# Kernel tuning notes

Measured on AMD Instinct MI355X. Metric: run time of the kernel, lower is better.

## Reference

```python
import jax, jax.numpy as jnp
import numpy as np

C = 128
B = 64
EPS = 1e-6


def _ln2d(x, w, b):
    # LayerNorm over channel dim (NAFNet-style LayerNorm2d), eps=1e-6
    mu = x.mean(axis=1, keepdims=True)
    var = ((x - mu) ** 2).mean(axis=1, keepdims=True)
    return (x - mu) / jnp.sqrt(var + EPS) * w[None, :, None, None] + b[None, :, None, None]


def _conv4(x, w, b):
    # Conv2d kernel 4, stride 4, no padding; NCHW / OIHW
    y = jax.lax.conv_general_dilated(x, w, (4, 4), 'VALID',
                                     dimension_numbers=('NCHW', 'OIHW', 'NCHW'))
    return y + b[None, :, None, None]


def _pixel_shuffle4(x):
    # (B, c*16, H, W) -> (B, c, 4H, 4W), torch PixelShuffle semantics
    b, c16, h, w = x.shape
    c = c16 // 16
    x = x.reshape(b, c, 4, 4, h, w)
    x = x.transpose(0, 1, 4, 2, 5, 3)
    return x.reshape(b, c, h * 4, w * 4)


def setup_inputs() -> dict:
    key = jax.random.key(0)
    ks = jax.random.split(key, 16)
    s = 0.02
    return {
        'x_l': jax.random.normal(ks[0], (B, C, 32, 32), jnp.float32),
        'x_r': jax.random.normal(ks[1], (B, C, 32, 32), jnp.float32),
        'ln_w_l': jnp.ones((C,), jnp.float32), 'ln_b_l': jnp.zeros((C,), jnp.float32),
        'ln_w_r': jnp.ones((C,), jnp.float32), 'ln_b_r': jnp.zeros((C,), jnp.float32),
        'Wl1': jax.random.normal(ks[2], (C, C, 4, 4), jnp.float32) * s,
        'bl1': jnp.zeros((C,), jnp.float32),
        'Wr1': jax.random.normal(ks[3], (C, C, 4, 4), jnp.float32) * s,
        'br1': jnp.zeros((C,), jnp.float32),
        'Wl2': jax.random.normal(ks[4], (C, C, 4, 4), jnp.float32) * s,
        'bl2': jnp.zeros((C,), jnp.float32),
        'Wr2': jax.random.normal(ks[5], (C, C, 4, 4), jnp.float32) * s,
        'br2': jnp.zeros((C,), jnp.float32),
        'pos': jax.random.normal(ks[6], (1, C, 8, 8), jnp.float32),
        'beta': jax.random.normal(ks[7], (1, C, 1, 1), jnp.float32) * s,
        'gamma': jax.random.normal(ks[8], (1, C, 1, 1), jnp.float32) * s,
        'Wl3': jax.random.normal(ks[9], (16 * C, C), jnp.float32) * s,
        'bl3': jnp.zeros((16 * C,), jnp.float32),
        'Wr3': jax.random.normal(ks[10], (16 * C, C), jnp.float32) * s,
        'br3': jnp.zeros((16 * C,), jnp.float32),
    }


def reference(x_l, x_r, ln_w_l, ln_b_l, ln_w_r, ln_b_r, Wl1, bl1, Wr1, br1,
              Wl2, bl2, Wr2, br2, pos, beta, gamma, Wl3, bl3, Wr3, br3):
    c = x_l.shape[1]
    scale = c ** (-0.5)
    B1 = x_l.shape[0]
    B2 = x_r.shape[0]

    Ql = _conv4(_ln2d(x_l, ln_w_l, ln_b_l), Wl1, bl1) + pos  # (B1,c,8,8)
    Qr = _conv4(_ln2d(x_r, ln_w_r, ln_b_r), Wr1, br1) + pos  # (B2,c,8,8)
    h1, w1 = Ql.shape[-2], Ql.shape[-1]
    h2, w2 = Qr.shape[-2], Qr.shape[-1]
    m1, m2 = h1 * w1, h2 * w2

    Qlm = Ql.transpose(0, 2, 3, 1).reshape(B1, m1, c)          # b (h w) c
    Qrm = Qr.transpose(1, 0, 2, 3).reshape(c, B2 * m2)         # c (b h w)
    Vl = (_conv4(x_l, Wl2, bl2) + pos).transpose(0, 2, 3, 1).reshape(B1 * m1, c)
    Vr = (_conv4(x_r, Wr2, br2) + pos).transpose(0, 2, 3, 1).reshape(B2 * m2, c)

    attn = jnp.matmul(Qlm, Qrm) * scale                        # (B1, m1, B2*m2)

    F_r2l = jnp.matmul(jax.nn.softmax(attn * (B2 ** (-0.5)), axis=-1), Vr)
    F_r2l = F_r2l.reshape(B1, h1, w1, c)

    attn2 = attn.reshape(B1, m1, B2, m2).transpose(2, 3, 0, 1).reshape(B2, m2, B1 * m1)
    F_l2r = jnp.matmul(jax.nn.softmax(attn2 * (B1 ** (-0.5)), axis=-1), Vl)
    F_l2r = F_l2r.reshape(B2, h2, w2, c)

    F_r2l = _pixel_shuffle4((jnp.matmul(F_r2l, Wl3.T) + bl3).transpose(0, 3, 1, 2)) * beta
    F_l2r = _pixel_shuffle4((jnp.matmul(F_l2r, Wr3.T) + br3).transpose(0, 3, 1, 2)) * gamma
    return (x_l + F_r2l, x_r + F_l2r)
```

## Files before the change

### kernel.cpp

```cpp
#include <hip/hip_runtime.h>
#include <stdint.h>

using bf16x8 = __attribute__((ext_vector_type(8))) short;
using f32x4  = __attribute__((ext_vector_type(4))) float;

__device__ __forceinline__ unsigned short f2bf(float f) {
  union { float f; uint32_t u; } v; v.f = f;
  uint32_t r = v.u + 0x7FFFu + ((v.u >> 16) & 1u);
  return (unsigned short)(r >> 16);
}
__device__ __forceinline__ uint32_t pk2(float a, float b) {
  return (uint32_t)f2bf(a) | ((uint32_t)f2bf(b) << 16);
}
__device__ __forceinline__ float bf2f(unsigned short s) {
  union { uint32_t u; float f; } v; v.u = ((uint32_t)s) << 16;
  return v.f;
}
__device__ __forceinline__ f32x4 mfma16(bf16x8 a, bf16x8 b, f32x4 c) {
  return __builtin_amdgcn_mfma_f32_16x16x32_bf16(a, b, c, 0, 0, 0);
}

__global__ __launch_bounds__(256) void k_lnstats(
    const float* __restrict__ xl, const float* __restrict__ xr,
    float* __restrict__ muW, float* __restrict__ rsW)
{
  const int bx = blockIdx.x;
  const int side = bx >> 7, rem = bx & 127;
  const int b = rem >> 1, half = rem & 1;
  const float* x = (side ? xr : xl) + (size_t)b * 131072 + half * 512;
  const int t = threadIdx.x;
  const int px = t * 2;
  float s0=0, s1=0, q0=0, q1=0;
#pragma unroll 4
  for (int c = 0; c < 128; ++c) {
    const float2 v = *(const float2*)(x + c*1024 + px);
    s0 += v.x; q0 += v.x*v.x;
    s1 += v.y; q1 += v.y*v.y;
  }
  const int o = (side*64 + b)*1024 + half*512 + px;
  float2 mu, rs;
  mu.x = s0*(1.0f/128.0f); mu.y = s1*(1.0f/128.0f);
  rs.x = rsqrtf(fmaxf(q0*(1.0f/128.0f) - mu.x*mu.x, 0.0f) + 1e-6f);
  rs.y = rsqrtf(fmaxf(q1*(1.0f/128.0f) - mu.y*mu.y, 0.0f) + 1e-6f);
  *(float2*)(muW + o) = mu;
  *(float2*)(rsW + o) = rs;
}

__global__ __launch_bounds__(256) void k_wprep(
    const float* __restrict__ lnwl, const float* __restrict__ lnbl,
    const float* __restrict__ lnwr, const float* __restrict__ lnbr,
    const float* __restrict__ Wl1, const float* __restrict__ bl1,
    const float* __restrict__ Wr1, const float* __restrict__ br1,
    const float* __restrict__ Wl2, const float* __restrict__ Wr2,
    unsigned short* __restrict__ Wq, unsigned short* __restrict__ Wv,
    float* __restrict__ bqW)
{
  const int bx = blockIdx.x;
  const int side = bx >> 7, co = bx & 127;
  const float* W1  = side ? Wr1 : Wl1;
  const float* W2  = side ? Wr2 : Wl2;
  const float* b1  = side ? br1 : bl1;
  const float* lnw = side ? lnwr : lnwl;
  const float* lnb = side ? lnbr : lnbl;
  const int t = threadIdx.x;
  const int ci = t >> 1;
  const float lw = lnw[ci], lb = lnb[ci];

  const size_t dsto = (size_t)(side*32 + (t>>3))*8192 + (size_t)co*64 + (t&7)*8;

  const float* src1 = W1 + (size_t)co*2048 + t*8;
  const float4 a0 = *(const float4*)(src1);
  const float4 a1 = *(const float4*)(src1 + 4);
  float part = (a0.x+a0.y+a0.z+a0.w + a1.x+a1.y+a1.z+a1.w) * lb;
  uint4 pkq;
  pkq.x = pk2(a0.x*lw, a0.y*lw); pkq.y = pk2(a0.z*lw, a0.w*lw);
  pkq.z = pk2(a1.x*lw, a1.y*lw); pkq.w = pk2(a1.z*lw, a1.w*lw);
  *(uint4*)(Wq + dsto) = pkq;

  const float* src2 = W2 + (size_t)co*2048 + t*8;
  const float4 c0 = *(const float4*)(src2);
  const float4 c1 = *(const float4*)(src2 + 4);
  uint4 pkv;
  pkv.x = pk2(c0.x, c0.y); pkv.y = pk2(c0.z, c0.w);
  pkv.z = pk2(c1.x, c1.y); pkv.w = pk2(c1.z, c1.w);
  *(uint4*)(Wv + dsto) = pkv;

  __shared__ float red[4];
  float v = part;
  v += __shfl_down(v, 32, 64); v += __shfl_down(v, 16, 64);
  v += __shfl_down(v, 8, 64);  v += __shfl_down(v, 4, 64);
  v += __shfl_down(v, 2, 64);  v += __shfl_down(v, 1, 64);
  if ((t & 63) == 0) red[t >> 6] = v;
  __syncthreads();
  if (t == 0) bqW[side*128 + co] = b1[co] + red[0] + red[1] + red[2] + red[3];
}

__global__ __launch_bounds__(256) void k_conv(
    const float* __restrict__ xl, const float* __restrict__ xr,
    const unsigned short* __restrict__ Wq, const unsigned short* __restrict__ Wv,
    const float* __restrict__ muW, const float* __restrict__ rsW,
    unsigned short* __restrict__ Cpart)
{
  const int bid = blockIdx.x;
  const int ks = bid & 3;
  const int img = (bid >> 2) & 63;
  const int ctype = bid >> 8;
  const int side = ctype & 1;
  const bool isQ = ctype < 2;
  const float* x = (side ? xr : xl) + (size_t)img * 131072;
  const unsigned short* Bsrc = (isQ ? Wq : Wv) + (size_t)side * 262144;

  const int t = threadIdx.x;
  const int w = t >> 6, l = t & 63, lo = l & 15, g = l >> 4;

  __shared__ __align__(16) unsigned char lds[24576];
  unsigned char* A = lds;
  unsigned char* B = lds + 8192;

  const int cl   = t >> 6;
  const int px0  = (t & 63) * 16;
  const int y    = px0 >> 5;
  const int wr   = y & 3;
  const int pbase = (y >> 2)*8 + ((px0 & 31) >> 2);

  float4 mu4[4], rs4[4];
  if (isQ) {
    const int o = (side*64 + img)*1024 + px0;
#pragma unroll
    for (int i = 0; i < 4; ++i) {
      mu4[i] = *(const float4*)(muW + o + 4*i);
      rs4[i] = *(const float4*)(rsW + o + 4*i);
    }
  }

  const int cout = t >> 1, part = t & 1;
  const int keyB = ((cout ^ (cout >> 3)) & 7) << 4;

  f32x4 acc[4][2];
#pragma unroll
  for (int a = 0; a < 4; ++a) { acc[a][0] = (f32x4)0.0f; acc[a][1] = (f32x4)0.0f; }

  for (int it = 0; it < 8; ++it) {
    const int kb = ks*8 + it;
    __syncthreads();
    {
      const float* xs = x + (size_t)(kb*4 + cl)*1024 + px0;
#pragma unroll
      for (int i = 0; i < 4; ++i) {
        float4 v = *(const float4*)(xs + 4*i);
        if (isQ) {
          v.x = (v.x - mu4[i].x)*rs4[i].x; v.y = (v.y - mu4[i].y)*rs4[i].y;
          v.z = (v.z - mu4[i].z)*rs4[i].z; v.w = (v.w - mu4[i].w)*rs4[i].w;
        }
        const int p = pbase + i;
        int dst = p*128 + cl*32 + wr*8;
        dst ^= ((p ^ (p >> 3)) & 7) << 4;
        *(uint2*)(A + dst) = make_uint2(pk2(v.x, v.y), pk2(v.z, v.w));
      }
    }
    {
      const unsigned short* bs = Bsrc + (size_t)kb*8192 + t*32;
#pragma unroll
      for (int i = 0; i < 4; ++i) {
        const bf16x8 v = *(const bf16x8*)(bs + i*8);
        *(bf16x8*)(B + cout*128 + ((part*64 + i*16) ^ keyB)) = v;
      }
    }
    __syncthreads();
    bf16x8 af[4][2], bfr[2][2];
#pragma unroll
    for (int mf = 0; mf < 4; ++mf) {
      const int row = mf*16 + lo;
      const int key = ((row ^ (row >> 3)) & 7) << 4;
#pragma unroll
      for (int kc = 0; kc < 2; ++kc)
        af[mf][kc] = *(const bf16x8*)(A + row*128 + ((kc*64 + g*16) ^ key));
    }
#pragma unroll
    for (int nf = 0; nf < 2; ++nf) {
      const int row = w*32 + nf*16 + lo;
      const int key = ((row ^ (row >> 3)) & 7) << 4;
#pragma unroll
      for (int kc = 0; kc < 2; ++kc)
        bfr[nf][kc] = *(const bf16x8*)(B + row*128 + ((kc*64 + g*16) ^ key));
    }
    __builtin_amdgcn_s_setprio(1);
#pragma unroll
    for (int kc = 0; kc < 2; ++kc)
#pragma unroll
      for (int nf = 0; nf < 2; ++nf)
#pragma unroll
        for (int mf = 0; mf < 4; ++mf)
          acc[mf][nf] = mfma16(af[mf][kc], bfr[nf][kc], acc[mf][nf]);
    __builtin_amdgcn_s_setprio(0);
  }

  unsigned short* Cp = Cpart + (size_t)bid * 8192;
#pragma unroll
  for (int mf = 0; mf < 4; ++mf)
#pragma unroll
    for (int nf = 0; nf < 2; ++nf) {
      const int c = w*32 + nf*16 + lo;
      const int p0 = mf*16 + g*4;
      *(uint2*)(Cp + c*64 + p0) =
          make_uint2(pk2(acc[mf][nf][0], acc[mf][nf][1]),
                     pk2(acc[mf][nf][2], acc[mf][nf][3]));
    }
}

__global__ __launch_bounds__(256) void k_convred(
    const unsigned short* __restrict__ Cpart,
    const float* __restrict__ bqW,
    const float* __restrict__ bl2, const float* __restrict__ br2,
    const float* __restrict__ pos,
    unsigned short* __restrict__ Qbf, unsigned short* __restrict__ Vtbf)
{
  const int bid2 = blockIdx.x;
  const int ctype = bid2 >> 6, img = bid2 & 63;
  const int side = ctype & 1;
  const bool isQ = ctype < 2;
  const int t = threadIdx.x;

  __shared__ float S[64][130];

  const int c = t >> 1, p0 = (t & 1) * 32;
  {
    float acc[32];
#pragma unroll
    for (int j = 0; j < 32; ++j) acc[j] = 0.f;
#pragma unroll
    for (int s = 0; s < 4; ++s) {
      const unsigned short* Cp = Cpart + ((size_t)(bid2*4 + s))*8192 + c*64 + p0;
#pragma unroll
      for (int j8 = 0; j8 < 4; ++j8) {
        const bf16x8 v = *(const bf16x8*)(Cp + j8*8);
#pragma unroll
        for (int e = 0; e < 8; ++e)
          acc[j8*8 + e] += bf2f((unsigned short)v[e]);
      }
    }
#pragma unroll
    for (int j = 0; j < 32; ++j) S[p0 + j][c] = acc[j];
  }
  __syncthreads();

  if (isQ) {
    const float* bq = bqW + side*128;
    const int p = t >> 2, c0 = (t & 3) * 32;
    const int rot = (t & 3) * 4;
    uint32_t pk[16];
#pragma unroll
    for (int j2 = 0; j2 < 16; ++j2) {
      const int jj = (j2 + rot) & 15;
      const int ca = c0 + jj*2;
      const float2 sv = *(const float2*)(&S[p][ca]);
      const float va = (sv.x + bq[ca]     + pos[ca*64 + p])     * 0.105112052f;
      const float vb = (sv.y + bq[ca + 1] + pos[(ca+1)*64 + p]) * 0.105112052f;
      pk[jj] = pk2(va, vb);
    }
    unsigned short* Qo = Qbf + (size_t)side*524288 + ((size_t)(img*64 + p))*128 + c0;
    *(uint4*)(Qo)      = make_uint4(pk[0],  pk[1],  pk[2],  pk[3]);
    *(uint4*)(Qo + 8)  = make_uint4(pk[4],  pk[5],  pk[6],  pk[7]);
    *(uint4*)(Qo + 16) = make_uint4(pk[8],  pk[9],  pk[10], pk[11]);
    *(uint4*)(Qo + 24) = make_uint4(pk[12], pk[13], pk[14], pk[15]);
  } else {
    const float* b2 = side ? br2 : bl2;
    const float bb = b2[c];
    uint32_t pk[16];
#pragma unroll
    for (int j2 = 0; j2 < 16; ++j2) {
      const int pa = p0 + j2*2;
      const float va = S[pa][c]     + bb + pos[c*64 + pa];
      const float vb = S[pa + 1][c] + bb + pos[c*64 + pa + 1];
      pk[j2] = pk2(va, vb);
    }
    unsigned short* Vo = Vtbf + (size_t)side*524288 + (size_t)c*4096 + img*64 + p0;
    *(uint4*)(Vo)      = make_uint4(pk[0],  pk[1],  pk[2],  pk[3]);
    *(uint4*)(Vo + 8)  = make_uint4(pk[4],  pk[5],  pk[6],  pk[7]);
    *(uint4*)(Vo + 16) = make_uint4(pk[8],  pk[9],  pk[10], pk[11]);
    *(uint4*)(Vo + 24) = make_uint4(pk[12], pk[13], pk[14], pk[15]);
  }
}

__global__ __launch_bounds__(256) void k_attn(
    const unsigned short* __restrict__ Qbf,
    const unsigned short* __restrict__ Vtbf,
    float* __restrict__ Opart,
    float* __restrict__ Lpart)
{
  const int qb = blockIdx.x, ks = blockIdx.y, dir = blockIdx.z;
  const unsigned short* Qp = Qbf  + (size_t)dir*524288;
  const unsigned short* Kp = Qbf  + (size_t)(1-dir)*524288;
  const unsigned short* Vp = Vtbf + (size_t)(1-dir)*524288;

  const int t = threadIdx.x;
  const int w = t >> 6, l = t & 63, lo = l & 15, g = l >> 4;

  __shared__ __align__(16) unsigned char ldsK[16384];
  __shared__ __align__(16) unsigned char ldsV[16384];
  __shared__ __align__(16) unsigned char ldsP[4096];
  __shared__ float lred[4][32];

  bf16x8 aq[2][4];
#pragma unroll
  for (int mf = 0; mf < 2; ++mf)
#pragma unroll
    for (int kc = 0; kc < 4; ++kc)
      aq[mf][kc] = *(const bf16x8*)(Qp + (size_t)(qb*32 + mf*16 + lo)*128 + kc*32 + g*8);

  f32x4 o[2][2];
  o[0][0]=(f32x4)0.0f; o[0][1]=(f32x4)0.0f; o[1][0]=(f32x4)0.0f; o[1][1]=(f32x4)0.0f;
  float ls[2][4] = {{0,0,0,0},{0,0,0,0}};

  const int kt0 = ks * 16;
  for (int it = 0; it < 16; ++it) {
    const int kt = kt0 + it;
    __syncthreads();
    {
      const uint4* src = (const uint4*)(Kp + (size_t)kt*8192);
#pragma unroll
      for (int j = 0; j < 4; ++j) {
        const int idx = t + 256*j;
        const int dst = idx*16;
        const int row = dst >> 8;
        *(uint4*)(ldsK + dst) = src[(dst ^ ((row & 7) << 4)) >> 4];
      }
#pragma unroll
      for (int j = 0; j < 4; ++j) {
        const int idx = t + 256*j;
        const int c = idx >> 3, i = idx & 7;
        const int inrow = (i*16) ^ ((c & 7) << 4);
        const uint4 v = *(const uint4*)(Vp + (size_t)c*4096 + kt*64 + (inrow >> 1));
        *(uint4*)(ldsV + c*128 + i*16) = v;
      }
    }
    __syncthreads();
    f32x4 s[2]; s[0] = (f32x4)0.0f; s[1] = (f32x4)0.0f;
    const int krow = w*16 + lo;
    __builtin_amdgcn_s_setprio(1);
#pragma unroll
    for (int kc = 0; kc < 4; ++kc) {
      const bf16x8 bk = *(const bf16x8*)(ldsK + krow*256 + ((kc*64 + g*16) ^ ((krow & 7) << 4)));
      s[0] = mfma16(aq[0][kc], bk, s[0]);
      s[1] = mfma16(aq[1][kc], bk, s[1]);
    }
    __builtin_amdgcn_s_setprio(0);
#pragma unroll
    for (int mf = 0; mf < 2; ++mf)
#pragma unroll
      for (int rr = 0; rr < 4; ++rr) {
        const float e = __expf(s[mf][rr]);
        ls[mf][rr] += e;
        const int q = mf*16 + g*4 + rr;
        const int inrow = (w*32 + lo*2) ^ ((q & 7) << 4);
        *(unsigned short*)(ldsP + q*128 + inrow) = f2bf(e);
      }
    __syncthreads();
    __builtin_amdgcn_s_setprio(1);
#pragma unroll
    for (int kd = 0; kd < 2; ++kd) {
      bf16x8 pa[2];
#pragma unroll
      for (int mf = 0; mf < 2; ++mf) {
        const int q = mf*16 + lo;
        pa[mf] = *(const bf16x8*)(ldsP + q*128 + ((kd*64 + g*16) ^ ((q & 7) << 4)));
      }
#pragma unroll
      for (int nf = 0; nf < 2; ++nf) {
        const int c = w*32 + nf*16 + lo;
        const bf16x8 bv = *(const bf16x8*)(ldsV + c*128 + ((kd*64 + g*16) ^ ((c & 7) << 4)));
        o[0][nf] = mfma16(pa[0], bv, o[0][nf]);
        o[1][nf] = mfma16(pa[1], bv, o[1][nf]);
      }
    }
    __builtin_amdgcn_s_setprio(0);
  }

#pragma unroll
  for (int mf = 0; mf < 2; ++mf)
#pragma unroll
    for (int rr = 0; rr < 4; ++rr) {
      float v = ls[mf][rr];
      v += __shfl_xor(v, 1, 64);
      v += __shfl_xor(v, 2, 64);
      v += __shfl_xor(v, 4, 64);
      v += __shfl_xor(v, 8, 64);
      ls[mf][rr] = v;
    }
  if (lo == 0) {
#pragma unroll
    for (int mf = 0; mf < 2; ++mf)
#pragma unroll
      for (int rr = 0; rr < 4; ++rr)
        lred[w][mf*16 + g*4 + rr] = ls[mf][rr];
  }
  __syncthreads();

  float* Ob = Opart + (((size_t)dir*128 + qb)*4 + ks)*32*128;
#pragma unroll
  for (int mf = 0; mf < 2; ++mf)
#pragma unroll
    for (int nf = 0; nf < 2; ++nf) {
      const int c = w*32 + nf*16 + lo;
#pragma unroll
      for (int rr = 0; rr < 4; ++rr) {
        const int q = mf*16 + g*4 + rr;
        Ob[q*128 + c] = o[mf][nf][rr];
      }
    }
  if (t < 32)
    Lpart[(((size_t)dir*128 + qb)*4 + ks)*32 + t] =
        lred[0][t] + lred[1][t] + lred[2][t] + lred[3][t];
}

__global__ __launch_bounds__(256) void k_reduce(
    const float* __restrict__ Opart, const float* __restrict__ Lpart,
    unsigned short* __restrict__ Fbf)
{
  const int bid = blockIdx.x;
  const int dir = bid >> 7, qb = bid & 127;
  const int t = threadIdx.x;
  const int qr = t >> 3;
  const int cs = (t & 7) * 16;
  const size_t pb = ((size_t)dir*128 + qb)*4;
  float acc[16];
#pragma unroll
  for (int i = 0; i < 16; ++i) acc[i] = 0.f;
  float lsum = 0.f;
#pragma unroll
  for (int s = 0; s < 4; ++s) {
    const float* Ob = Opart + ((pb + s)*32 + qr)*128 + cs;
#pragma unroll
    for (int i = 0; i < 16; i += 4) {
      const float4 v = *(const float4*)(Ob + i);
      acc[i] += v.x; acc[i+1] += v.y; acc[i+2] += v.z; acc[i+3] += v.w;
    }
    lsum += Lpart[(pb + s)*32 + qr];
  }
  const float inv = 1.0f / lsum;
  uint32_t pkw[8];
#pragma unroll
  for (int i = 0; i < 8; ++i) pkw[i] = pk2(acc[2*i]*inv, acc[2*i+1]*inv);
  unsigned short* Fo = Fbf + (size_t)dir*524288 + ((size_t)qb*32 + qr)*128 + cs;
  *(uint4*)(Fo)     = make_uint4(pkw[0], pkw[1], pkw[2], pkw[3]);
  *(uint4*)(Fo + 8) = make_uint4(pkw[4], pkw[5], pkw[6], pkw[7]);
}

__global__ __launch_bounds__(256) void k_proj(
    const unsigned short* __restrict__ Fbf,
    const float* __restrict__ Wl3, const float* __restrict__ bl3,
    const float* __restrict__ Wr3, const float* __restrict__ br3,
    const float* __restrict__ beta, const float* __restrict__ gamma,
    const float* __restrict__ xl, const float* __restrict__ xr,
    float* __restrict__ out)
{
  const int nb = blockIdx.x, mb = blockIdx.y, side = blockIdx.z;
  const unsigned short* F = Fbf + (size_t)side*524288;
  const float* W3  = side ? Wr3 : Wl3;
  const float* b3  = side ? br3 : bl3;
  const float* scl = side ? gamma : beta;
  const float* xin = side ? xr : xl;
  float* op = out + (size_t)side*8388608;

  const int t = threadIdx.x;
  const int w = t >> 6, l = t & 63, lo = l & 15, g = l >> 4;

  __shared__ __align__(16) unsigned char Ft[16384];
  __shared__ __align__(16) unsigned char B3[32768];

  {
    const uint4* src = (const uint4*)(F + (size_t)mb*8192);
#pragma unroll
    for (int j = 0; j < 4; ++j) {
      const int idx = t + 256*j;
      const int dst = idx*16;
      const int row = dst >> 8;
      *(uint4*)(Ft + dst) = src[(dst ^ ((row & 7) << 4)) >> 4];
    }
  }
  {
    const int nl = t >> 1, half = t & 1;
    const float* wsrc = W3 + (size_t)(nb*128 + nl)*128 + half*64;
#pragma unroll
    for (int ch = 0; ch < 8; ++ch) {
      const float4 v0 = *(const float4*)(wsrc + ch*8);
      const float4 v1 = *(const float4*)(wsrc + ch*8 + 4);
      uint4 pk;
      pk.x = pk2(v0.x,v0.y); pk.y = pk2(v0.z,v0.w);
      pk.z = pk2(v1.x,v1.y); pk.w = pk2(v1.z,v1.w);
      const int inrow = (half*128 + ch*16) ^ ((nl & 7) << 4);
      *(uint4*)(B3 + nl*256 + inrow) = pk;
    }
  }
  __syncthreads();

  f32x4 acc[4][2];
#pragma unroll
  for (int a=0;a<4;a++) { acc[a][0] = (f32x4)0.0f; acc[a][1] = (f32x4)0.0f; }

  bf16x8 af[4][4];
#pragma unroll
  for (int mf = 0; mf < 4; ++mf) {
    const int row = mf*16 + lo;
#pragma unroll
    for (int kc = 0; kc < 4; ++kc)
      af[mf][kc] = *(const bf16x8*)(Ft + row*256 + ((kc*64 + g*16) ^ ((row & 7) << 4)));
  }
#pragma unroll
  for (int kc = 0; kc < 4; ++kc)
#pragma unroll
    for (int nf = 0; nf < 2; ++nf) {
      const int n = w*32 + nf*16 + lo;
      const bf16x8 bb = *(const bf16x8*)(B3 + n*256 + ((kc*64 + g*16) ^ ((n & 7) << 4)));
#pragma unroll
      for (int mf = 0; mf < 4; ++mf)
        acc[mf][nf] = mfma16(af[mf][kc], bb, acc[mf][nf]);
    }

#pragma unroll
  for (int mf = 0; mf < 4; ++mf)
#pragma unroll
    for (int nf = 0; nf < 2; ++nf) {
      const int n16 = nb*128 + w*32 + nf*16 + lo;
      const int c = n16 >> 4, r4 = (n16 >> 2) & 3, sc = n16 & 3;
      const float scc = scl[c];
      const float bb3 = b3[n16];
#pragma unroll
      for (int rr = 0; rr < 4; ++rr) {
        const int pi = mf*16 + g*4 + rr;
        const int h = pi >> 3, wc = pi & 7;
        const size_t oidx = ((size_t)(mb*128 + c))*1024 + (size_t)(h*4 + r4)*32 + wc*4 + sc;
        op[oidx] = xin[oidx] + scc*(acc[mf][nf][rr] + bb3);
      }
    }
}

extern "C" void kernel_launch(void* const* d_in, const int* in_sizes, int n_in,
                              void* d_out, int out_size, void* d_ws, size_t ws_size,
                              hipStream_t stream) {
  (void)in_sizes; (void)n_in; (void)out_size; (void)ws_size;
  const float* xl   = (const float*)d_in[0];
  const float* xr   = (const float*)d_in[1];
  const float* lnwl = (const float*)d_in[2];
  const float* lnbl = (const float*)d_in[3];
  const float* lnwr = (const float*)d_in[4];
  const float* lnbr = (const float*)d_in[5];
  const float* Wl1  = (const float*)d_in[6];
  const float* bl1  = (const float*)d_in[7];
  const float* Wr1  = (const float*)d_in[8];
  const float* br1  = (const float*)d_in[9];
  const float* Wl2  = (const float*)d_in[10];
  const float* bl2  = (const float*)d_in[11];
  const float* Wr2  = (const float*)d_in[12];
  const float* br2  = (const float*)d_in[13];
  const float* pos  = (const float*)d_in[14];
  const float* beta = (const float*)d_in[15];
  const float* gamma= (const float*)d_in[16];
  const float* Wl3  = (const float*)d_in[17];
  const float* bl3  = (const float*)d_in[18];
  const float* Wr3  = (const float*)d_in[19];
  const float* br3  = (const float*)d_in[20];

  float* muW = (float*)d_ws;
  float* rsW = muW + 131072;
  float* bqW = rsW + 131072;
  unsigned short* Wq   = (unsigned short*)(bqW + 256);
  unsigned short* Wv   = Wq + 524288;
  unsigned short* Qbf  = Wv + 524288;
  unsigned short* Vtbf = Qbf + 1048576;
  unsigned short* Fbf  = Vtbf + 1048576;
  unsigned short* Cpart = Fbf + 1048576;
  float* Opart = (float*)Cpart;
  float* Lpart = (float*)(Cpart + 8388608);

  k_lnstats<<<256, 256, 0, stream>>>(xl, xr, muW, rsW);
  k_wprep<<<256, 256, 0, stream>>>(lnwl, lnbl, lnwr, lnbr,
      Wl1, bl1, Wr1, br1, Wl2, Wr2, Wq, Wv, bqW);
  k_conv<<<1024, 256, 0, stream>>>(xl, xr, Wq, Wv, muW, rsW, Cpart);
  k_convred<<<256, 256, 0, stream>>>(Cpart, bqW, bl2, br2, pos, Qbf, Vtbf);
  k_attn<<<dim3(128, 4, 2), 256, 0, stream>>>(Qbf, Vtbf, Opart, Lpart);
  k_reduce<<<256, 256, 0, stream>>>(Opart, Lpart, Fbf);
  k_proj<<<dim3(16, 64, 2), 256, 0, stream>>>(Fbf, Wl3, bl3, Wr3, br3,
      beta, gamma, xl, xr, (float*)d_out);
}
```

Measured before the change: 148.8 us.

## Double-buffer K/V tiles and double query rows per attention block

The attention kernel now processes 64 query rows per block instead of 32, halving the grid and reusing each loaded K/V tile across twice as many MFMAs. K/V tiles for the next iteration are prefetched into registers before compute and written into a second LDS buffer afterwards, which removes one barrier per iteration and overlaps global loads with math. The reduce kernel is reindexed to the new partial layout. This raises LDS use to about 73KB and register pressure, and halves the block count to 512, which may limit occupancy.

```diff
diff --git a/kernel.cpp b/kernel.cpp
--- a/kernel.cpp
+++ b/kernel.cpp
@@ -282,7 +282,7 @@
   }
 }
 
-__global__ __launch_bounds__(256) void k_attn(
+__global__ __launch_bounds__(256, 2) void k_attn(
     const unsigned short* __restrict__ Qbf,
     const unsigned short* __restrict__ Vtbf,
     float* __restrict__ Opart,
@@ -296,57 +296,79 @@
   const int t = threadIdx.x;
   const int w = t >> 6, l = t & 63, lo = l & 15, g = l >> 4;
 
-  __shared__ __align__(16) unsigned char ldsK[16384];
-  __shared__ __align__(16) unsigned char ldsV[16384];
-  __shared__ __align__(16) unsigned char ldsP[4096];
-  __shared__ float lred[4][32];
-
-  bf16x8 aq[2][4];
-#pragma unroll
-  for (int mf = 0; mf < 2; ++mf)
+  __shared__ __align__(16) unsigned char lds[73728];
+  unsigned char* ldsP = lds + 65536;
+  __shared__ float lred[4][64];
+
+  bf16x8 aq[4][4];
+#pragma unroll
+  for (int mf = 0; mf < 4; ++mf)
 #pragma unroll
     for (int kc = 0; kc < 4; ++kc)
-      aq[mf][kc] = *(const bf16x8*)(Qp + (size_t)(qb*32 + mf*16 + lo)*128 + kc*32 + g*8);
-
-  f32x4 o[2][2];
-  o[0][0]=(f32x4)0.0f; o[0][1]=(f32x4)0.0f; o[1][0]=(f32x4)0.0f; o[1][1]=(f32x4)0.0f;
-  float ls[2][4] = {{0,0,0,0},{0,0,0,0}};
+      aq[mf][kc] = *(const bf16x8*)(Qp + (size_t)(qb*64 + mf*16 + lo)*128 + kc*32 + g*8);
+
+  f32x4 o[4][2];
+#pragma unroll
+  for (int a = 0; a < 4; ++a) { o[a][0] = (f32x4)0.0f; o[a][1] = (f32x4)0.0f; }
+  float ls[4][4] = {{0,0,0,0},{0,0,0,0},{0,0,0,0},{0,0,0,0}};
 
   const int kt0 = ks * 16;
+
+  const int ksrcBase = t ^ ((t >> 4) & 7);
+  const int vc    = t >> 3;
+  const int vi16  = (t & 7) * 16;
+  const int vsoff = (vi16 ^ (((t >> 3) & 7) << 4)) >> 1;
+
+  {
+    const uint4* src = (const uint4*)(Kp + (size_t)kt0*8192);
+#pragma unroll
+    for (int j = 0; j < 4; ++j)
+      *(uint4*)(lds + (t + 256*j)*16) = src[ksrcBase + 256*j];
+#pragma unroll
+    for (int j = 0; j < 4; ++j) {
+      const int c = vc + 32*j;
+      *(uint4*)(lds + 32768 + c*128 + vi16) =
+          *(const uint4*)(Vp + (size_t)c*4096 + kt0*64 + vsoff);
+    }
+  }
+  __syncthreads();
+
   for (int it = 0; it < 16; ++it) {
-    const int kt = kt0 + it;
-    __syncthreads();
-    {
+    const int cur = it & 1;
+    unsigned char* curK = lds + cur*16384;
+    unsigned char* curV = lds + 32768 + cur*16384;
+
+    uint4 kr0, kr1, kr2, kr3, vr0, vr1, vr2, vr3;
+    if (it < 15) {
+      const int kt = kt0 + it + 1;
       const uint4* src = (const uint4*)(Kp + (size_t)kt*8192);
-#pragma unroll
-      for (int j = 0; j < 4; ++j) {
-        const int idx = t + 256*j;
-        const int dst = idx*16;
-        const int row = dst >> 8;
-        *(uint4*)(ldsK + dst) = src[(dst ^ ((row & 7) << 4)) >> 4];
-      }
-#pragma unroll
-      for (int j = 0; j < 4; ++j) {
-        const int idx = t + 256*j;
-        const int c = idx >> 3, i = idx & 7;
-        const int inrow = (i*16) ^ ((c & 7) << 4);
-        const uint4 v = *(const uint4*)(Vp + (size_t)c*4096 + kt*64 + (inrow >> 1));
-        *(uint4*)(ldsV + c*128 + i*16) = v;
-      }
-    }
-    __syncthreads();
-    f32x4 s[2]; s[0] = (f32x4)0.0f; s[1] = (f32x4)0.0f;
+      kr0 = src[ksrcBase];
+      kr1 = src[ksrcBase + 256];
+      kr2 = src[ksrcBase + 512];
+      kr3 = src[ksrcBase + 768];
+      const unsigned short* vsrc = Vp + (size_t)kt*64 + vsoff;
+      vr0 = *(const uint4*)(vsrc + (size_t)(vc     )*4096);
+      vr1 = *(const uint4*)(vsrc + (size_t)(vc + 32)*4096);
+      vr2 = *(const uint4*)(vsrc + (size_t)(vc + 64)*4096);
+      vr3 = *(const uint4*)(vsrc + (size_t)(vc + 96)*4096);
+    }
+
+    f32x4 s[4];
+    s[0] = (f32x4)0.0f; s[1] = (f32x4)0.0f; s[2] = (f32x4)0.0f; s[3] = (f32x4)0.0f;
     const int krow = w*16 + lo;
+    const int keyk = (krow & 7) << 4;
     __builtin_amdgcn_s_setprio(1);
 #pragma unroll
     for (int kc = 0; kc < 4; ++kc) {
-      const bf16x8 bk = *(const bf16x8*)(ldsK + krow*256 + ((kc*64 + g*16) ^ ((krow & 7) << 4)));
-      s[0] = mfma16(aq[0][kc], bk, s[0]);
-      s[1] = mfma16(aq[1][kc], bk, s[1]);
+      const bf16x8 bk = *(const bf16x8*)(curK + krow*256 + ((kc*64 + g*16) ^ keyk));
+#pragma unroll
+      for (int mf = 0; mf < 4; ++mf)
+        s[mf] = mfma16(aq[mf][kc], bk, s[mf]);
     }
     __builtin_amdgcn_s_setprio(0);
-#pragma unroll
-    for (int mf = 0; mf < 2; ++mf)
+
+#pragma unroll
+    for (int mf = 0; mf < 4; ++mf)
 #pragma unroll
       for (int rr = 0; rr < 4; ++rr) {
         const float e = __expf(s[mf][rr]);
@@ -356,28 +378,44 @@
         *(unsigned short*)(ldsP + q*128 + inrow) = f2bf(e);
       }
     __syncthreads();
+
     __builtin_amdgcn_s_setprio(1);
 #pragma unroll
     for (int kd = 0; kd < 2; ++kd) {
-      bf16x8 pa[2];
-#pragma unroll
-      for (int mf = 0; mf < 2; ++mf) {
+      bf16x8 pa[4];
+#pragma unroll
+      for (int mf = 0; mf < 4; ++mf) {
         const int q = mf*16 + lo;
         pa[mf] = *(const bf16x8*)(ldsP + q*128 + ((kd*64 + g*16) ^ ((q & 7) << 4)));
       }
 #pragma unroll
       for (int nf = 0; nf < 2; ++nf) {
         const int c = w*32 + nf*16 + lo;
-        const bf16x8 bv = *(const bf16x8*)(ldsV + c*128 + ((kd*64 + g*16) ^ ((c & 7) << 4)));
-        o[0][nf] = mfma16(pa[0], bv, o[0][nf]);
-        o[1][nf] = mfma16(pa[1], bv, o[1][nf]);
+        const bf16x8 bv = *(const bf16x8*)(curV + c*128 + ((kd*64 + g*16) ^ ((c & 7) << 4)));
+#pragma unroll
+        for (int mf = 0; mf < 4; ++mf)
+          o[mf][nf] = mfma16(pa[mf], bv, o[mf][nf]);
       }
     }
     __builtin_amdgcn_s_setprio(0);
-  }
-
-#pragma unroll
-  for (int mf = 0; mf < 2; ++mf)
+
+    if (it < 15) {
+      unsigned char* nK = lds + (cur ^ 1)*16384;
+      unsigned char* nV = lds + 32768 + (cur ^ 1)*16384;
+      *(uint4*)(nK + (t      )*16) = kr0;
+      *(uint4*)(nK + (t + 256)*16) = kr1;
+      *(uint4*)(nK + (t + 512)*16) = kr2;
+      *(uint4*)(nK + (t + 768)*16) = kr3;
+      *(uint4*)(nV + (vc     )*128 + vi16) = vr0;
+      *(uint4*)(nV + (vc + 32)*128 + vi16) = vr1;
+      *(uint4*)(nV + (vc + 64)*128 + vi16) = vr2;
+      *(uint4*)(nV + (vc + 96)*128 + vi16) = vr3;
+    }
+    __syncthreads();
+  }
+
+#pragma unroll
+  for (int mf = 0; mf < 4; ++mf)
 #pragma unroll
     for (int rr = 0; rr < 4; ++rr) {
       float v = ls[mf][rr];
@@ -389,16 +427,16 @@
     }
   if (lo == 0) {
 #pragma unroll
-    for (int mf = 0; mf < 2; ++mf)
+    for (int mf = 0; mf < 4; ++mf)
 #pragma unroll
       for (int rr = 0; rr < 4; ++rr)
         lred[w][mf*16 + g*4 + rr] = ls[mf][rr];
   }
   __syncthreads();
 
-  float* Ob = Opart + (((size_t)dir*128 + qb)*4 + ks)*32*128;
-#pragma unroll
-  for (int mf = 0; mf < 2; ++mf)
+  float* Ob = Opart + (((size_t)dir*64 + qb)*4 + ks)*64*128;
+#pragma unroll
+  for (int mf = 0; mf < 4; ++mf)
 #pragma unroll
     for (int nf = 0; nf < 2; ++nf) {
       const int c = w*32 + nf*16 + lo;
@@ -408,8 +446,8 @@
         Ob[q*128 + c] = o[mf][nf][rr];
       }
     }
-  if (t < 32)
-    Lpart[(((size_t)dir*128 + qb)*4 + ks)*32 + t] =
+  if (t < 64)
+    Lpart[(((size_t)dir*64 + qb)*4 + ks)*64 + t] =
         lred[0][t] + lred[1][t] + lred[2][t] + lred[3][t];
 }
 
@@ -418,30 +456,32 @@
     unsigned short* __restrict__ Fbf)
 {
   const int bid = blockIdx.x;
-  const int dir = bid >> 7, qb = bid & 127;
+  const int dir = bid >> 7, rb = bid & 127;
   const int t = threadIdx.x;
   const int qr = t >> 3;
   const int cs = (t & 7) * 16;
-  const size_t pb = ((size_t)dir*128 + qb)*4;
+  const int r  = rb*32 + qr;
+  const int qb = r >> 6, q = r & 63;
+  const size_t pb = ((size_t)dir*64 + qb)*4;
   float acc[16];
 #pragma unroll
   for (int i = 0; i < 16; ++i) acc[i] = 0.f;
   float lsum = 0.f;
 #pragma unroll
   for (int s = 0; s < 4; ++s) {
-    const float* Ob = Opart + ((pb + s)*32 + qr)*128 + cs;
+    const float* Ob = Opart + ((pb + s)*64 + q)*128 + cs;
 #pragma unroll
     for (int i = 0; i < 16; i += 4) {
       const float4 v = *(const float4*)(Ob + i);
       acc[i] += v.x; acc[i+1] += v.y; acc[i+2] += v.z; acc[i+3] += v.w;
     }
-    lsum += Lpart[(pb + s)*32 + qr];
+    lsum += Lpart[(pb + s)*64 + q];
   }
   const float inv = 1.0f / lsum;
   uint32_t pkw[8];
 #pragma unroll
   for (int i = 0; i < 8; ++i) pkw[i] = pk2(acc[2*i]*inv, acc[2*i+1]*inv);
-  unsigned short* Fo = Fbf + (size_t)dir*524288 + ((size_t)qb*32 + qr)*128 + cs;
+  unsigned short* Fo = Fbf + (size_t)dir*524288 + (size_t)r*128 + cs;
   *(uint4*)(Fo)     = make_uint4(pkw[0], pkw[1], pkw[2], pkw[3]);
   *(uint4*)(Fo + 8) = make_uint4(pkw[4], pkw[5], pkw[6], pkw[7]);
 }
@@ -578,7 +618,7 @@
       Wl1, bl1, Wr1, br1, Wl2, Wr2, Wq, Wv, bqW);
   k_conv<<<1024, 256, 0, stream>>>(xl, xr, Wq, Wv, muW, rsW, Cpart);
   k_convred<<<256, 256, 0, stream>>>(Cpart, bqW, bl2, br2, pos, Qbf, Vtbf);
-  k_attn<<<dim3(128, 4, 2), 256, 0, stream>>>(Qbf, Vtbf, Opart, Lpart);
+  k_attn<<<dim3(64, 4, 2), 256, 0, stream>>>(Qbf, Vtbf, Opart, Lpart);
   k_reduce<<<256, 256, 0, stream>>>(Opart, Lpart, Fbf);
   k_proj<<<dim3(16, 64, 2), 256, 0, stream>>>(Fbf, Wl3, bl3, Wr3, br3,
       beta, gamma, xl, xr, (float*)d_out);
```

Measured after the change: 135.8 us. 1.1x faster.
